# Kernel optimization log

Measured on AMD Instinct MI355X. Metric: run time of the kernel, lower is better.

## Reference

```python
import jax, jax.numpy as jnp
import numpy as np

N, T, C, G, E = 50000, 2, 768, 16, 800000
H = C // 4          # 192
OUT = 3
EPS = 1e-5


def _lin_init(k, fan_in, fan_out):
    s = 1.0 / np.sqrt(fan_in)
    kw, kb = jax.random.split(k)
    W = jax.random.uniform(kw, (fan_in, fan_out), minval=-s, maxval=s, dtype=jnp.float32)
    b = jax.random.uniform(kb, (fan_out,), minval=-s, maxval=s, dtype=jnp.float32)
    return W, b


def setup_inputs() -> dict:
    key = jax.random.key(0)
    ks = jax.random.split(key, 8)
    x = jax.random.normal(ks[0], (N, T, C), dtype=jnp.float32)
    batch = jnp.sort(jax.random.randint(ks[1], (N,), 0, G))
    edge_index = jax.random.randint(ks[2], (2, E), 0, N)
    W0, b0 = _lin_init(ks[3], C, H)
    W1, b1 = _lin_init(ks[4], H, H)
    Wh1, bh1 = _lin_init(ks[5], H, H)
    Wh2, bh2 = _lin_init(ks[6], H, OUT)
    ones = jnp.ones((H,), jnp.float32)
    zeros = jnp.zeros((H,), jnp.float32)
    return {
        "x": x, "batch": batch, "edge_index": edge_index,
        "W0": W0, "b0": b0, "gn0_w": ones, "gn0_b": zeros, "gn0_a": ones,
        "W1": W1, "b1": b1, "gn1_w": ones, "gn1_b": zeros, "gn1_a": ones,
        "Wh1": Wh1, "bh1": bh1, "Wh2": Wh2, "bh2": bh2,
    }


def _gelu(v):
    return jax.nn.gelu(v, approximate=False)  # torch nn.GELU default = exact erf


def _gcn_conv(h, W, b, src, dst, dinv):
    # PyG GCNConv: x' = D^-1/2 (A+I) D^-1/2 (x W) + b, self-loops added implicitly
    h = jnp.einsum('ntc,cd->ntd', h, W)                       # [N,T,Cout]
    norm = (dinv[src] * dinv[dst])[:, None, None]             # [E,1,1]
    agg = jax.ops.segment_sum(h[src] * norm, dst, num_segments=N)
    agg = agg + h * (dinv * dinv)[:, None, None]              # self-loop term
    return agg + b


def _graph_norm(h, batch, cnt, w, b, alpha):
    # PyG GraphNorm: per-graph mean/var with learnable mean scale
    mean = jax.ops.segment_sum(h, batch, num_segments=G) / cnt   # [G,T,C]
    out = h - alpha * mean[batch]
    var = jax.ops.segment_sum(out * out, batch, num_segments=G) / cnt
    std = jnp.sqrt(var + EPS)
    return w * out / std[batch] + b


def reference(x, batch, edge_index,
              W0, b0, gn0_w, gn0_b, gn0_a,
              W1, b1, gn1_w, gn1_b, gn1_a,
              Wh1, bh1, Wh2, bh2):
    src, dst = edge_index[0], edge_index[1]
    deg = jax.ops.segment_sum(jnp.ones((E,), jnp.float32), dst, num_segments=N) + 1.0
    dinv = jax.lax.rsqrt(deg)
    cnt = jax.ops.segment_sum(jnp.ones((N,), jnp.float32), batch, num_segments=G)[:, None, None]

    # layer 0: 768 -> 192 (no residual, shape mismatch)
    h = _gcn_conv(x, W0, b0, src, dst, dinv)
    h = _gelu(_graph_norm(h, batch, cnt, gn0_w, gn0_b, gn0_a))
    # layer 1: 192 -> 192 with residual
    h_in = h
    h = _gcn_conv(h, W1, b1, src, dst, dinv)
    h = _gelu(_graph_norm(h, batch, cnt, gn1_w, gn1_b, gn1_a))
    h = h + h_in
    # MLP head
    h = _gelu(jnp.einsum('ntc,cd->ntd', h, Wh1) + bh1)
    out = jnp.einsum('ntc,cd->ntd', h, Wh2) + bh2            # [N,T,3]
    return out
```

## Files before the change

### kernel.cpp

```cpp
#include <hip/hip_runtime.h>
#include <math.h>

#define NN   50000
#define TT   2
#define CC   768
#define GG   16
#define EE   800000
#define HH   192
#define OUTD 3
#define MR   (NN*TT)
#define FD   (TT*HH)
#define EPS_GN 1e-5f
#define GN_CHUNK 32
#define AGG_CH 128

typedef __attribute__((ext_vector_type(8))) short bf16x8;
typedef __attribute__((ext_vector_type(4))) float f32x4;

__device__ __forceinline__ float gelu_exact(float x){
    return 0.5f * x * (1.0f + erff(x * 0.70710678118654752440f));
}

__device__ __forceinline__ short f2b(float f){
    unsigned u = __float_as_uint(f);
    unsigned r = (u + 0x7FFFu + ((u>>16)&1u)) >> 16;
    return (short)r;
}
__device__ __forceinline__ float b2f(unsigned short u){
    return __uint_as_float(((unsigned)u)<<16);
}

__global__ __launch_bounds__(256) void k_deg(const int* __restrict__ dst, float* __restrict__ deg){
    int e = blockIdx.x*256 + threadIdx.x;
    if(e < EE) atomicAdd(&deg[dst[e]], 1.0f);
}

__global__ __launch_bounds__(64) void k_cnt2(const int* __restrict__ batch, float* __restrict__ cnt){
    int g = threadIdx.x;
    if(g >= GG) return;
    int lo0=0, hi=NN;
    while(lo0<hi){ int mid=(lo0+hi)>>1; if(batch[mid] < g) lo0=mid+1; else hi=mid; }
    int lo1=lo0; hi=NN;
    while(lo1<hi){ int mid=(lo1+hi)>>1; if(batch[mid] < g+1) lo1=mid+1; else hi=mid; }
    cnt[g] = (float)(lo1 - lo0);
}

__global__ __launch_bounds__(256) void k_wconv(const float* __restrict__ W0, const float* __restrict__ W1,
                                               const float* __restrict__ Wh1,
                                               short* __restrict__ Wt0, short* __restrict__ Wt1,
                                               short* __restrict__ Wth1){
    int i = blockIdx.x*256 + threadIdx.x;
    if(i < CC*HH){
        int k = i / HH, n = i % HH;
        Wt0[(size_t)n*CC + k] = f2b(W0[i]);
    }
    if(i < HH*HH){
        int k = i / HH, n = i % HH;
        Wt1 [(size_t)n*HH + k] = f2b(W1[i]);
        Wth1[(size_t)n*HH + k] = f2b(Wh1[i]);
    }
}

__global__ __launch_bounds__(256) void k_scan1(const float* __restrict__ deg, int* __restrict__ partial,
                                               float* __restrict__ dinv){
    __shared__ int s[256];
    int t = threadIdx.x;
    int i = blockIdx.x*256 + t;
    float dv = (i < NN) ? deg[i] : 0.f;
    if(i < NN) dinv[i] = rsqrtf(dv + 1.0f);
    int v = (int)dv;
    s[t] = v; __syncthreads();
    for(int off=128; off>0; off>>=1){ if(t < off) s[t] += s[t+off]; __syncthreads(); }
    if(t == 0) partial[blockIdx.x] = s[0];
}

__global__ __launch_bounds__(256) void k_scan2(int* __restrict__ partial){
    __shared__ int s[256];
    int t = threadIdx.x;
    int v = partial[t];
    s[t] = v; __syncthreads();
    for(int off=1; off<256; off<<=1){
        int x = (t >= off) ? s[t-off] : 0;
        __syncthreads();
        s[t] += x;
        __syncthreads();
    }
    partial[t] = s[t] - v;
}

__global__ __launch_bounds__(256) void k_scan3(const float* __restrict__ deg, const int* __restrict__ partial,
                                               int* __restrict__ csr_off){
    __shared__ int s[256];
    int t = threadIdx.x;
    int i = blockIdx.x*256 + t;
    int v = (i < NN) ? (int)deg[i] : 0;
    s[t] = v; __syncthreads();
    for(int off=1; off<256; off<<=1){
        int x = (t >= off) ? s[t-off] : 0;
        __syncthreads();
        s[t] += x;
        __syncthreads();
    }
    if(i < NN) csr_off[i] = partial[blockIdx.x] + s[t] - v;
}

__global__ __launch_bounds__(256) void k_fill(const int* __restrict__ src, const int* __restrict__ dst,
                                              const int* __restrict__ csr_off, int* __restrict__ fillcnt,
                                              int* __restrict__ csr_src){
    int e = blockIdx.x*256 + threadIdx.x;
    if(e < EE){
        int d = dst[e];
        int pos = csr_off[d] + atomicAdd(&fillcnt[d], 1);
        csr_src[pos] = src[e];
    }
}

__device__ __forceinline__ void gn8r(float4 u0, float4 u1,
                                     const float* __restrict__ sm, const float* __restrict__ sq,
                                     int sb, int hb_,
                                     const float* __restrict__ wg, const float* __restrict__ bg,
                                     const float* __restrict__ ag, float ic, float v[8]){
    float4 m0 = *(const float4*)(sm+sb),   m1 = *(const float4*)(sm+sb+4);
    float4 q0 = *(const float4*)(sq+sb),   q1 = *(const float4*)(sq+sb+4);
    float4 w0 = *(const float4*)(wg+hb_),  w1 = *(const float4*)(wg+hb_+4);
    float4 b0 = *(const float4*)(bg+hb_),  b1 = *(const float4*)(bg+hb_+4);
    float4 a0 = *(const float4*)(ag+hb_),  a1 = *(const float4*)(ag+hb_+4);
    float uu[8]={u0.x,u0.y,u0.z,u0.w,u1.x,u1.y,u1.z,u1.w};
    float mm[8]={m0.x,m0.y,m0.z,m0.w,m1.x,m1.y,m1.z,m1.w};
    float qq[8]={q0.x,q0.y,q0.z,q0.w,q1.x,q1.y,q1.z,q1.w};
    float ww[8]={w0.x,w0.y,w0.z,w0.w,w1.x,w1.y,w1.z,w1.w};
    float bb[8]={b0.x,b0.y,b0.z,b0.w,b1.x,b1.y,b1.z,b1.w};
    float aa[8]={a0.x,a0.y,a0.z,a0.w,a1.x,a1.y,a1.z,a1.w};
    #pragma unroll
    for(int j=0;j<8;j++){
        float mean = mm[j]*ic, ex2 = qq[j]*ic, al = aa[j];
        float var = ex2 - (2.0f*al - al*al)*mean*mean;
        float t = ww[j]*(uu[j] - al*mean)*rsqrtf(var + EPS_GN) + bb[j];
        v[j] = gelu_exact(t);
    }
}

template<int MODE, int NORM, bool BIAS>
__global__ __launch_bounds__(256) void k_gemm_mfma(
        const float* __restrict__ A1, const float* __restrict__ A0,
        const short* __restrict__ Bt,
        const float* __restrict__ bias, void* __restrict__ Cv,
        const float* __restrict__ W2, const float* __restrict__ b2,
        const int* __restrict__ batch, const float* __restrict__ cnt,
        const float* __restrict__ sm1, const float* __restrict__ sq1,
        const float* __restrict__ wg1, const float* __restrict__ bg1, const float* __restrict__ ag1,
        const float* __restrict__ sm0, const float* __restrict__ sq0,
        const float* __restrict__ wg0, const float* __restrict__ bg0, const float* __restrict__ ag0,
        int Mrows, int Kdim){
    __shared__ short As[64][40];
    __shared__ short Bs[192][40];
    int tid = threadIdx.x;
    int bm = blockIdx.x*64;
    int wv = tid>>6, lane = tid&63;
    int lm = lane&15, lq = lane>>4;

    f32x4 acc[12];
    #pragma unroll
    for(int i=0;i<12;i++) acc[i] = (f32x4){0.f,0.f,0.f,0.f};

    int ar = tid>>2, akg = (tid&3)<<3;
    int row = bm + ar;
    bool aok = row < Mrows;
    const float* Ap1 = A1 + (size_t)row*Kdim + akg;
    const float* Ap0 = (NORM==2) ? (A0 + (size_t)row*Kdim + akg) : nullptr;
    int g = 0, tT = 0; float ic = 0.f;
    if(NORM >= 1 && aok){
        int nn = row>>1; tT = row&1;
        g = batch[nn];
        ic = 1.0f / cnt[g];
    }

    float4 ra0 = make_float4(0,0,0,0), ra1 = ra0, rb0 = ra0, rb1 = ra0;
    bf16x8 bv[3];
    if(aok){
        ra0 = *(const float4*)(Ap1); ra1 = *(const float4*)(Ap1 + 4);
        if(NORM==2){ rb0 = *(const float4*)(Ap0); rb1 = *(const float4*)(Ap0 + 4); }
    }
    #pragma unroll
    for(int i=0;i<3;i++){
        int idx = tid + i*256;
        int n = idx>>2, kg = (idx&3)<<3;
        bv[i] = *(const bf16x8*)(Bt + (size_t)n*Kdim + kg);
    }

    for(int k0 = 0; k0 < Kdim; k0 += 32){
        bf16x8 ap = {};
        if(aok){
            if(NORM == 0){
                ap[0]=f2b(ra0.x); ap[1]=f2b(ra0.y); ap[2]=f2b(ra0.z); ap[3]=f2b(ra0.w);
                ap[4]=f2b(ra1.x); ap[5]=f2b(ra1.y); ap[6]=f2b(ra1.z); ap[7]=f2b(ra1.w);
            } else {
                int hb_ = akg + k0;
                int sb  = g*FD + tT*HH + hb_;
                float v[8];
                gn8r(ra0, ra1, sm1, sq1, sb, hb_, wg1, bg1, ag1, ic, v);
                if(NORM == 2){
                    float v0[8];
                    gn8r(rb0, rb1, sm0, sq0, sb, hb_, wg0, bg0, ag0, ic, v0);
                    #pragma unroll
                    for(int j=0;j<8;j++) v[j] += v0[j];
                }
                #pragma unroll
                for(int j=0;j<8;j++) ap[j] = f2b(v[j]);
            }
        }
        bf16x8 bw0 = bv[0], bw1 = bv[1], bw2 = bv[2];
        __syncthreads();
        *(bf16x8*)&As[ar][akg] = ap;
        {
            int idx0 = tid, idx1 = tid+256, idx2 = tid+512;
            *(bf16x8*)&Bs[idx0>>2][(idx0&3)<<3] = bw0;
            *(bf16x8*)&Bs[idx1>>2][(idx1&3)<<3] = bw1;
            *(bf16x8*)&Bs[idx2>>2][(idx2&3)<<3] = bw2;
        }
        __syncthreads();
        int k1 = k0 + 32;
        if(k1 < Kdim){
            if(aok){
                ra0 = *(const float4*)(Ap1 + k1); ra1 = *(const float4*)(Ap1 + k1 + 4);
                if(NORM==2){ rb0 = *(const float4*)(Ap0 + k1); rb1 = *(const float4*)(Ap0 + k1 + 4); }
            }
            #pragma unroll
            for(int i=0;i<3;i++){
                int idx = tid + i*256;
                int n = idx>>2, kg = (idx&3)<<3;
                bv[i] = *(const bf16x8*)(Bt + (size_t)n*Kdim + k1 + kg);
            }
        }
        bf16x8 af = *(const bf16x8*)&As[wv*16 + lm][lq*8];
        #pragma unroll
        for(int ct=0; ct<12; ct++){
            bf16x8 bfr = *(const bf16x8*)&Bs[ct*16 + lm][lq*8];
            acc[ct] = __builtin_amdgcn_mfma_f32_16x16x32_bf16(af, bfr, acc[ct], 0, 0, 0);
        }
    }

    if(MODE == 1){
        short* C = (short*)Cv;
        #pragma unroll
        for(int ct=0; ct<12; ct++){
            int col = ct*16 + lm;
            float bs = BIAS ? bias[col] : 0.f;
            #pragma unroll
            for(int r=0; r<4; r++){
                int orow = bm + wv*16 + lq*4 + r;
                if(orow < Mrows) C[(size_t)orow*HH + col] = f2b(acc[ct][r] + bs);
            }
        }
    } else {
        float hs[4][3] = {};
        #pragma unroll
        for(int ct=0; ct<12; ct++){
            int col = ct*16 + lm;
            float bs = bias[col];
            float w20 = W2[col*3+0], w21 = W2[col*3+1], w22 = W2[col*3+2];
            #pragma unroll
            for(int r=0; r<4; r++){
                float gl = gelu_exact(acc[ct][r] + bs);
                hs[r][0] += gl*w20; hs[r][1] += gl*w21; hs[r][2] += gl*w22;
            }
        }
        #pragma unroll
        for(int off=1; off<16; off<<=1){
            #pragma unroll
            for(int r=0;r<4;r++){
                hs[r][0] += __shfl_xor(hs[r][0], off);
                hs[r][1] += __shfl_xor(hs[r][1], off);
                hs[r][2] += __shfl_xor(hs[r][2], off);
            }
        }
        if(lm == 0){
            float* O = (float*)Cv;
            #pragma unroll
            for(int r=0;r<4;r++){
                int orow = bm + wv*16 + lq*4 + r;
                if(orow < Mrows){
                    O[(size_t)orow*3+0] = hs[r][0] + b2[0];
                    O[(size_t)orow*3+1] = hs[r][1] + b2[1];
                    O[(size_t)orow*3+2] = hs[r][2] + b2[2];
                }
            }
        }
    }
}

__global__ __launch_bounds__(192) void k_agg(const ushort* __restrict__ hw, const int* __restrict__ csr_src,
                                             const int* __restrict__ csr_off, const float* __restrict__ deg,
                                             const float* __restrict__ dinv, const float* __restrict__ bias,
                                             float* __restrict__ out){
    __shared__ int   sidx[AGG_CH];
    __shared__ float swt [AGG_CH];
    int n = blockIdx.x;
    int t = threadIdx.x;
    float di = dinv[n];
    const ushort2* H2 = (const ushort2*)hw;
    ushort2 sv = H2[(size_t)n*192 + t];
    float self = di*di;
    float ax = b2f(sv.x)*self, ay = b2f(sv.y)*self;
    int beg = csr_off[n];
    int end = beg + (int)deg[n];
    for(int base = beg; base < end; base += AGG_CH){
        int m = min(AGG_CH, end - base);
        __syncthreads();
        for(int j = t; j < m; j += 192){
            int s = csr_src[base + j];
            sidx[j] = s;
            swt[j] = dinv[s]*di;
        }
        __syncthreads();
        int j = 0;
        for(; j+8 <= m; j += 8){
            int   si[8]; float wt[8]; ushort2 vv[8];
            #pragma unroll
            for(int q=0;q<8;q++){ si[q]=sidx[j+q]; wt[q]=swt[j+q]; }
            #pragma unroll
            for(int q=0;q<8;q++) vv[q] = H2[(size_t)si[q]*192 + t];
            #pragma unroll
            for(int q=0;q<8;q++){ ax += wt[q]*b2f(vv[q].x); ay += wt[q]*b2f(vv[q].y); }
        }
        for(; j < m; j++){
            int s = sidx[j]; float ww = swt[j];
            ushort2 v = H2[(size_t)s*192 + t];
            ax += ww*b2f(v.x); ay += ww*b2f(v.y);
        }
    }
    int f = 2*t;
    int hh = (f < HH) ? f : f - HH;
    out[(size_t)n*FD + f]   = ax + bias[hh];
    out[(size_t)n*FD + f+1] = ay + bias[hh+1];
}

__global__ __launch_bounds__(384) void k_gn_stats(const float* __restrict__ h, const int* __restrict__ batch,
                                                  float* __restrict__ ssum, float* __restrict__ ssq){
    int f = threadIdx.x;
    int n0 = blockIdx.x*GN_CHUNK;
    int n1 = min(n0 + GN_CHUNK, NN);
    int g = batch[n0];
    float a = 0.f, a2 = 0.f;
    int n = n0;
    for(; n+4 <= n1; n += 4){
        float v0 = h[(size_t)n*FD + f];
        float v1 = h[(size_t)(n+1)*FD + f];
        float v2 = h[(size_t)(n+2)*FD + f];
        float v3 = h[(size_t)(n+3)*FD + f];
        int b3 = batch[n+3];
        if(b3 == g){
            a  += v0+v1+v2+v3;
            a2 += v0*v0+v1*v1+v2*v2+v3*v3;
        } else {
            float vv[4] = {v0,v1,v2,v3};
            #pragma unroll
            for(int q=0;q<4;q++){
                int gn = batch[n+q];
                if(gn != g){
                    atomicAdd(&ssum[g*FD + f], a);
                    atomicAdd(&ssq [g*FD + f], a2);
                    a = 0.f; a2 = 0.f; g = gn;
                }
                a += vv[q]; a2 += vv[q]*vv[q];
            }
        }
    }
    for(; n < n1; n++){
        int gn = batch[n];
        if(gn != g){
            atomicAdd(&ssum[g*FD + f], a);
            atomicAdd(&ssq [g*FD + f], a2);
            a = 0.f; a2 = 0.f; g = gn;
        }
        float v = h[(size_t)n*FD + f];
        a += v; a2 += v*v;
    }
    atomicAdd(&ssum[g*FD + f], a);
    atomicAdd(&ssq [g*FD + f], a2);
}

extern "C" void kernel_launch(void* const* d_in, const int* in_sizes, int n_in,
                              void* d_out, int out_size, void* d_ws, size_t ws_size,
                              hipStream_t stream){
    const float* x     = (const float*)d_in[0];
    const int*   batch = (const int*)d_in[1];
    const int*   ei    = (const int*)d_in[2];
    const int*   src   = ei;
    const int*   dst   = ei + EE;
    const float* W0    = (const float*)d_in[3];
    const float* b0    = (const float*)d_in[4];
    const float* gn0_w = (const float*)d_in[5];
    const float* gn0_b = (const float*)d_in[6];
    const float* gn0_a = (const float*)d_in[7];
    const float* W1    = (const float*)d_in[8];
    const float* b1    = (const float*)d_in[9];
    const float* gn1_w = (const float*)d_in[10];
    const float* gn1_b = (const float*)d_in[11];
    const float* gn1_a = (const float*)d_in[12];
    const float* Wh1   = (const float*)d_in[13];
    const float* bh1   = (const float*)d_in[14];
    const float* Wh2   = (const float*)d_in[15];
    const float* bh2   = (const float*)d_in[16];
    float* out = (float*)d_out;

    char* w = (char*)d_ws;
    auto alloc = [&](size_t bytes)->void*{
        void* p = (void*)w;
        w += (bytes + 255) & ~(size_t)255;
        return p;
    };
    char* zbase = w;
    float* deg     = (float*)alloc((size_t)NN*4);
    int*   fillcnt = (int*)  alloc((size_t)NN*4);
    int*   partial = (int*)  alloc(256*4);
    float* s0m     = (float*)alloc((size_t)GG*FD*4);
    float* s0q     = (float*)alloc((size_t)GG*FD*4);
    float* s1m     = (float*)alloc((size_t)GG*FD*4);
    float* s1q     = (float*)alloc((size_t)GG*FD*4);
    size_t zbytes = (size_t)(w - zbase);
    float* cnt     = (float*)alloc((size_t)GG*4);
    float* dinv    = (float*)alloc((size_t)NN*4);
    int*   csr_off = (int*)  alloc((size_t)NN*4);
    int*   csr_src = (int*)  alloc((size_t)EE*4);
    short* Wt0     = (short*)alloc((size_t)HH*CC*2);
    short* Wt1     = (short*)alloc((size_t)HH*HH*2);
    short* Wth1    = (short*)alloc((size_t)HH*HH*2);
    short* hb0     = (short*)alloc((size_t)MR*HH*2);
    short* hb1     = (short*)alloc((size_t)MR*HH*2);
    float* agg0    = (float*)alloc((size_t)MR*HH*4);
    float* agg1    = (float*)alloc((size_t)MR*HH*4);

    hipMemsetAsync(zbase, 0, zbytes, stream);

    k_deg  <<<(EE+255)/256, 256, 0, stream>>>(dst, deg);
    k_cnt2 <<<1, 64, 0, stream>>>(batch, cnt);
    k_wconv<<<(CC*HH+255)/256, 256, 0, stream>>>(W0, W1, Wh1, Wt0, Wt1, Wth1);

    int nscan = (NN+255)/256;
    k_scan1<<<nscan, 256, 0, stream>>>(deg, partial, dinv);
    k_scan2<<<1,     256, 0, stream>>>(partial);
    k_scan3<<<nscan, 256, 0, stream>>>(deg, partial, csr_off);
    k_fill <<<(EE+255)/256, 256, 0, stream>>>(src, dst, csr_off, fillcnt, csr_src);

    int gemm_grid = (MR+63)/64;
    int ngn = (NN + GN_CHUNK - 1)/GN_CHUNK;

    k_gemm_mfma<1,0,false><<<gemm_grid, 256, 0, stream>>>(
        x, nullptr, Wt0, nullptr, hb0, nullptr, nullptr,
        nullptr, nullptr,
        nullptr, nullptr, nullptr, nullptr, nullptr,
        nullptr, nullptr, nullptr, nullptr, nullptr, MR, CC);
    k_agg<<<NN, 192, 0, stream>>>((const ushort*)hb0, csr_src, csr_off, deg, dinv, b0, agg0);
    k_gn_stats<<<ngn, 384, 0, stream>>>(agg0, batch, s0m, s0q);

    k_gemm_mfma<1,1,false><<<gemm_grid, 256, 0, stream>>>(
        agg0, nullptr, Wt1, nullptr, hb1, nullptr, nullptr,
        batch, cnt,
        s0m, s0q, gn0_w, gn0_b, gn0_a,
        nullptr, nullptr, nullptr, nullptr, nullptr, MR, HH);
    k_agg<<<NN, 192, 0, stream>>>((const ushort*)hb1, csr_src, csr_off, deg, dinv, b1, agg1);
    k_gn_stats<<<ngn, 384, 0, stream>>>(agg1, batch, s1m, s1q);

    k_gemm_mfma<2,2,true><<<gemm_grid, 256, 0, stream>>>(
        agg1, agg0, Wth1, bh1, out, Wh2, bh2,
        batch, cnt,
        s1m, s1q, gn1_w, gn1_b, gn1_a,
        s0m, s0q, gn0_w, gn0_b, gn0_a, MR, HH);
}
```

Measured before the change: 985.9 us.

## Rework aggregation to warp-per-node with shuffles and restructure GEMMs

The aggregation kernel now gives each node one 64-lane wavefront instead of a 192-thread block. Edge indices and weights are broadcast with shuffles rather than staged through shared memory, and each lane handles six features. The 192-K GEMM now stages half of the weight matrix in LDS per phase and feeds A fragments straight from registers, which removes the per-k-step A staging and barriers. The 768-K GEMM is split into a dedicated kernel, and the group-count kernel is merged into the scan kernel to save one launch. The trade-offs are more scattered 4-byte gathers per lane in aggregation and a larger LDS footprint in the GEMM.

New measurement: 1.296 ms. 1.31x slower.

```diff
diff --git a/kernel.cpp b/kernel.cpp
--- a/kernel.cpp
+++ b/kernel.cpp
@@ -12,7 +12,6 @@
 #define FD   (TT*HH)
 #define EPS_GN 1e-5f
 #define GN_CHUNK 32
-#define AGG_CH 128
 
 typedef __attribute__((ext_vector_type(8))) short bf16x8;
 typedef __attribute__((ext_vector_type(4))) float f32x4;
@@ -33,16 +32,6 @@
 __global__ __launch_bounds__(256) void k_deg(const int* __restrict__ dst, float* __restrict__ deg){
     int e = blockIdx.x*256 + threadIdx.x;
     if(e < EE) atomicAdd(&deg[dst[e]], 1.0f);
-}
-
-__global__ __launch_bounds__(64) void k_cnt2(const int* __restrict__ batch, float* __restrict__ cnt){
-    int g = threadIdx.x;
-    if(g >= GG) return;
-    int lo0=0, hi=NN;
-    while(lo0<hi){ int mid=(lo0+hi)>>1; if(batch[mid] < g) lo0=mid+1; else hi=mid; }
-    int lo1=lo0; hi=NN;
-    while(lo1<hi){ int mid=(lo1+hi)>>1; if(batch[mid] < g+1) lo1=mid+1; else hi=mid; }
-    cnt[g] = (float)(lo1 - lo0);
 }
 
 __global__ __launch_bounds__(256) void k_wconv(const float* __restrict__ W0, const float* __restrict__ W1,
@@ -74,9 +63,18 @@
     if(t == 0) partial[blockIdx.x] = s[0];
 }
 
-__global__ __launch_bounds__(256) void k_scan2(int* __restrict__ partial){
+__global__ __launch_bounds__(256) void k_scan2(int* __restrict__ partial, const int* __restrict__ batch,
+                                               float* __restrict__ cnt){
     __shared__ int s[256];
     int t = threadIdx.x;
+    if(t < GG){
+        int g = t;
+        int lo0=0, hi=NN;
+        while(lo0<hi){ int mid=(lo0+hi)>>1; if(batch[mid] < g) lo0=mid+1; else hi=mid; }
+        int lo1=lo0; hi=NN;
+        while(lo1<hi){ int mid=(lo1+hi)>>1; if(batch[mid] < g+1) lo1=mid+1; else hi=mid; }
+        cnt[g] = (float)(lo1 - lo0);
+    }
     int v = partial[t];
     s[t] = v; __syncthreads();
     for(int off=1; off<256; off<<=1){
@@ -140,8 +138,81 @@
     }
 }
 
+__global__ __launch_bounds__(256) void k_gemm0(const float* __restrict__ A, const short* __restrict__ Bt,
+                                               short* __restrict__ C, int Mrows){
+    __shared__ short As[64][40];
+    __shared__ short Bs[192][40];
+    int tid = threadIdx.x;
+    int bm = blockIdx.x*64;
+    int wv = tid>>6, lane = tid&63;
+    int lm = lane&15, lq = lane>>4;
+
+    f32x4 acc[12];
+    #pragma unroll
+    for(int i=0;i<12;i++) acc[i] = (f32x4){0.f,0.f,0.f,0.f};
+
+    int ar = tid>>2, akg = (tid&3)<<3;
+    int row = bm + ar;
+    bool aok = row < Mrows;
+    const float* Ap = A + (size_t)row*CC + akg;
+
+    float4 ra0 = make_float4(0,0,0,0), ra1 = ra0;
+    bf16x8 bv[3];
+    if(aok){ ra0 = *(const float4*)(Ap); ra1 = *(const float4*)(Ap + 4); }
+    #pragma unroll
+    for(int i=0;i<3;i++){
+        int idx = tid + i*256;
+        int n = idx>>2, kg = (idx&3)<<3;
+        bv[i] = *(const bf16x8*)(Bt + (size_t)n*CC + kg);
+    }
+
+    for(int k0 = 0; k0 < CC; k0 += 32){
+        bf16x8 ap = {};
+        if(aok){
+            ap[0]=f2b(ra0.x); ap[1]=f2b(ra0.y); ap[2]=f2b(ra0.z); ap[3]=f2b(ra0.w);
+            ap[4]=f2b(ra1.x); ap[5]=f2b(ra1.y); ap[6]=f2b(ra1.z); ap[7]=f2b(ra1.w);
+        }
+        bf16x8 bw0 = bv[0], bw1 = bv[1], bw2 = bv[2];
+        __syncthreads();
+        *(bf16x8*)&As[ar][akg] = ap;
+        {
+            int idx0 = tid, idx1 = tid+256, idx2 = tid+512;
+            *(bf16x8*)&Bs[idx0>>2][(idx0&3)<<3] = bw0;
+            *(bf16x8*)&Bs[idx1>>2][(idx1&3)<<3] = bw1;
+            *(bf16x8*)&Bs[idx2>>2][(idx2&3)<<3] = bw2;
+        }
+        __syncthreads();
+        int k1 = k0 + 32;
+        if(k1 < CC){
+            if(aok){ ra0 = *(const float4*)(Ap + k1); ra1 = *(const float4*)(Ap + k1 + 4); }
+            #pragma unroll
+            for(int i=0;i<3;i++){
+                int idx = tid + i*256;
+                int n = idx>>2, kg = (idx&3)<<3;
+                bv[i] = *(const bf16x8*)(Bt + (size_t)n*CC + k1 + kg);
+            }
+        }
+        bf16x8 af = *(const bf16x8*)&As[wv*16 + lm][lq*8];
+        #pragma unroll
+        for(int ct=0; ct<12; ct++){
+            bf16x8 bfr = *(const bf16x8*)&Bs[ct*16 + lm][lq*8];
+            acc[ct] = __builtin_amdgcn_mfma_f32_16x16x32_bf16(af, bfr, acc[ct], 0, 0, 0);
+        }
+    }
+
+    #pragma unroll
+    for(int ct=0; ct<12; ct++){
+        int col = ct*16 + lm;
+        #pragma unroll
+        for(int r=0; r<4; r++){
+            int orow = bm + wv*16 + lq*4 + r;
+            if(orow < Mrows) C[(size_t)orow*HH + col] = f2b(acc[ct][r]);
+        }
+    }
+}
+
 template<int MODE, int NORM, bool BIAS>
-__global__ __launch_bounds__(256) void k_gemm_mfma(
+__global__ __launch_bounds__(256) void k_gemm192(
         const float* __restrict__ A1, const float* __restrict__ A0,
         const short* __restrict__ Bt,
         const float* __restrict__ bias, void* __restrict__ Cv,
@@ -151,9 +222,8 @@
         const float* __restrict__ wg1, const float* __restrict__ bg1, const float* __restrict__ ag1,
         const float* __restrict__ sm0, const float* __restrict__ sq0,
         const float* __restrict__ wg0, const float* __restrict__ bg0, const float* __restrict__ ag0,
-        int Mrows, int Kdim){
-    __shared__ short As[64][40];
-    __shared__ short Bs[192][40];
+        int Mrows){
+    __shared__ short Bs[192][104];
     int tid = threadIdx.x;
     int bm = blockIdx.x*64;
     int wv = tid>>6, lane = tid&63;
@@ -163,80 +233,62 @@
     #pragma unroll
     for(int i=0;i<12;i++) acc[i] = (f32x4){0.f,0.f,0.f,0.f};
 
-    int ar = tid>>2, akg = (tid&3)<<3;
-    int row = bm + ar;
+    int row = bm + wv*16 + lm;
     bool aok = row < Mrows;
-    const float* Ap1 = A1 + (size_t)row*Kdim + akg;
-    const float* Ap0 = (NORM==2) ? (A0 + (size_t)row*Kdim + akg) : nullptr;
+    const float* Ap1 = A1 + (size_t)row*HH + lq*8;
+    const float* Ap0 = (NORM==2) ? (A0 + (size_t)row*HH + lq*8) : nullptr;
     int g = 0, tT = 0; float ic = 0.f;
-    if(NORM >= 1 && aok){
-        int nn = row>>1; tT = row&1;
-        g = batch[nn];
+    if(aok){
+        g = batch[row>>1]; tT = row&1;
         ic = 1.0f / cnt[g];
     }
 
-    float4 ra0 = make_float4(0,0,0,0), ra1 = ra0, rb0 = ra0, rb1 = ra0;
-    bf16x8 bv[3];
-    if(aok){
-        ra0 = *(const float4*)(Ap1); ra1 = *(const float4*)(Ap1 + 4);
-        if(NORM==2){ rb0 = *(const float4*)(Ap0); rb1 = *(const float4*)(Ap0 + 4); }
-    }
-    #pragma unroll
-    for(int i=0;i<3;i++){
-        int idx = tid + i*256;
-        int n = idx>>2, kg = (idx&3)<<3;
-        bv[i] = *(const bf16x8*)(Bt + (size_t)n*Kdim + kg);
-    }
-
-    for(int k0 = 0; k0 < Kdim; k0 += 32){
-        bf16x8 ap = {};
-        if(aok){
-            if(NORM == 0){
-                ap[0]=f2b(ra0.x); ap[1]=f2b(ra0.y); ap[2]=f2b(ra0.z); ap[3]=f2b(ra0.w);
-                ap[4]=f2b(ra1.x); ap[5]=f2b(ra1.y); ap[6]=f2b(ra1.z); ap[7]=f2b(ra1.w);
-            } else {
-                int hb_ = akg + k0;
+    #pragma unroll
+    for(int ph=0; ph<2; ph++){
+        if(ph) __syncthreads();
+        #pragma unroll
+        for(int t=0;t<9;t++){
+            int idx = tid + t*256;
+            int n = idx/12, kg = (idx%12)*8;
+            *(bf16x8*)&Bs[n][kg] = *(const bf16x8*)(Bt + (size_t)n*HH + ph*96 + kg);
+        }
+        __syncthreads();
+        float4 pa[3][2], pb[3][2];
+        #pragma unroll
+        for(int k3=0;k3<3;k3++){
+            int k0 = ph*96 + k3*32;
+            if(aok){
+                pa[k3][0] = *(const float4*)(Ap1 + k0);
+                pa[k3][1] = *(const float4*)(Ap1 + k0 + 4);
+                if(NORM==2){
+                    pb[k3][0] = *(const float4*)(Ap0 + k0);
+                    pb[k3][1] = *(const float4*)(Ap0 + k0 + 4);
+                }
+            }
+        }
+        #pragma unroll
+        for(int k3=0;k3<3;k3++){
+            int k0 = ph*96 + k3*32;
+            bf16x8 ap = {};
+            if(aok){
+                int hb_ = k0 + lq*8;
                 int sb  = g*FD + tT*HH + hb_;
                 float v[8];
-                gn8r(ra0, ra1, sm1, sq1, sb, hb_, wg1, bg1, ag1, ic, v);
+                gn8r(pa[k3][0], pa[k3][1], sm1, sq1, sb, hb_, wg1, bg1, ag1, ic, v);
                 if(NORM == 2){
                     float v0[8];
-                    gn8r(rb0, rb1, sm0, sq0, sb, hb_, wg0, bg0, ag0, ic, v0);
+                    gn8r(pb[k3][0], pb[k3][1], sm0, sq0, sb, hb_, wg0, bg0, ag0, ic, v0);
                     #pragma unroll
                     for(int j=0;j<8;j++) v[j] += v0[j];
                 }
                 #pragma unroll
                 for(int j=0;j<8;j++) ap[j] = f2b(v[j]);
             }
-        }
-        bf16x8 bw0 = bv[0], bw1 = bv[1], bw2 = bv[2];
-        __syncthreads();
-        *(bf16x8*)&As[ar][akg] = ap;
-        {
-            int idx0 = tid, idx1 = tid+256, idx2 = tid+512;
-            *(bf16x8*)&Bs[idx0>>2][(idx0&3)<<3] = bw0;
-            *(bf16x8*)&Bs[idx1>>2][(idx1&3)<<3] = bw1;
-            *(bf16x8*)&Bs[idx2>>2][(idx2&3)<<3] = bw2;
-        }
-        __syncthreads();
-        int k1 = k0 + 32;
-        if(k1 < Kdim){
-            if(aok){
-                ra0 = *(const float4*)(Ap1 + k1); ra1 = *(const float4*)(Ap1 + k1 + 4);
-                if(NORM==2){ rb0 = *(const float4*)(Ap0 + k1); rb1 = *(const float4*)(Ap0 + k1 + 4); }
-            }
-            #pragma unroll
-            for(int i=0;i<3;i++){
-                int idx = tid + i*256;
-                int n = idx>>2, kg = (idx&3)<<3;
-                bv[i] = *(const bf16x8*)(Bt + (size_t)n*Kdim + k1 + kg);
-            }
-        }
-        bf16x8 af = *(const bf16x8*)&As[wv*16 + lm][lq*8];
-        #pragma unroll
-        for(int ct=0; ct<12; ct++){
-            bf16x8 bfr = *(const bf16x8*)&Bs[ct*16 + lm][lq*8];
-            acc[ct] = __builtin_amdgcn_mfma_f32_16x16x32_bf16(af, bfr, acc[ct], 0, 0, 0);
+            #pragma unroll
+            for(int ct=0; ct<12; ct++){
+                bf16x8 bfr = *(const bf16x8*)&Bs[ct*16 + lm][k3*32 + lq*8];
+                acc[ct] = __builtin_amdgcn_mfma_f32_16x16x32_bf16(ap, bfr, acc[ct], 0, 0, 0);
+            }
         }
     }
 
@@ -289,50 +341,62 @@
     }
 }
 
-__global__ __launch_bounds__(192) void k_agg(const ushort* __restrict__ hw, const int* __restrict__ csr_src,
+__global__ __launch_bounds__(256) void k_agg(const ushort* __restrict__ hw, const int* __restrict__ csr_src,
                                              const int* __restrict__ csr_off, const float* __restrict__ deg,
                                              const float* __restrict__ dinv, const float* __restrict__ bias,
                                              float* __restrict__ out){
-    __shared__ int   sidx[AGG_CH];
-    __shared__ float swt [AGG_CH];
-    int n = blockIdx.x;
-    int t = threadIdx.x;
+    int lane = threadIdx.x & 63;
+    int n = blockIdx.x*4 + (threadIdx.x>>6);
+    if(n >= NN) return;
     float di = dinv[n];
     const ushort2* H2 = (const ushort2*)hw;
-    ushort2 sv = H2[(size_t)n*192 + t];
+    size_t rb = (size_t)n*192 + lane*3;
+    ushort2 s0v = H2[rb], s1v = H2[rb+1], s2v = H2[rb+2];
     float self = di*di;
-    float ax = b2f(sv.x)*self, ay = b2f(sv.y)*self;
+    float a0 = b2f(s0v.x)*self, a1 = b2f(s0v.y)*self;
+    float a2 = b2f(s1v.x)*self, a3 = b2f(s1v.y)*self;
+    float a4 = b2f(s2v.x)*self, a5 = b2f(s2v.y)*self;
     int beg = csr_off[n];
     int end = beg + (int)deg[n];
-    for(int base = beg; base < end; base += AGG_CH){
-        int m = min(AGG_CH, end - base);
-        __syncthreads();
-        for(int j = t; j < m; j += 192){
-            int s = csr_src[base + j];
-            sidx[j] = s;
-            swt[j] = dinv[s]*di;
-        }
-        __syncthreads();
+    for(int base = beg; base < end; base += 64){
+        int m = min(64, end - base);
+        int e = 0; float we = 0.f;
+        if(lane < m){ e = csr_src[base + lane]; we = dinv[e]*di; }
         int j = 0;
-        for(; j+8 <= m; j += 8){
-            int   si[8]; float wt[8]; ushort2 vv[8];
-            #pragma unroll
-            for(int q=0;q<8;q++){ si[q]=sidx[j+q]; wt[q]=swt[j+q]; }
-            #pragma unroll
-            for(int q=0;q<8;q++) vv[q] = H2[(size_t)si[q]*192 + t];
-            #pragma unroll
-            for(int q=0;q<8;q++){ ax += wt[q]*b2f(vv[q].x); ay += wt[q]*b2f(vv[q].y); }
+        for(; j+4 <= m; j += 4){
+            int   sA=__shfl(e,j),  sB=__shfl(e,j+1),  sC=__shfl(e,j+2),  sD=__shfl(e,j+3);
+            float wA=__shfl(we,j), wB=__shfl(we,j+1), wC=__shfl(we,j+2), wD=__shfl(we,j+3);
+            size_t bA=(size_t)sA*192+lane*3, bB=(size_t)sB*192+lane*3;
+            size_t bC=(size_t)sC*192+lane*3, bD=(size_t)sD*192+lane*3;
+            ushort2 vA0=H2[bA], vA1=H2[bA+1], vA2=H2[bA+2];
+            ushort2 vB0=H2[bB], vB1=H2[bB+1], vB2=H2[bB+2];
+            ushort2 vC0=H2[bC], vC1=H2[bC+1], vC2=H2[bC+2];
+            ushort2 vD0=H2[bD], vD1=H2[bD+1], vD2=H2[bD+2];
+            a0 += wA*b2f(vA0.x)+wB*b2f(vB0.x)+wC*b2f(vC0.x)+wD*b2f(vD0.x);
+            a1 += wA*b2f(vA0.y)+wB*b2f(vB0.y)+wC*b2f(vC0.y)+wD*b2f(vD0.y);
+            a2 += wA*b2f(vA1.x)+wB*b2f(vB1.x)+wC*b2f(vC1.x)+wD*b2f(vD1.x);
+            a3 += wA*b2f(vA1.y)+wB*b2f(vB1.y)+wC*b2f(vC1.y)+wD*b2f(vD1.y);
+            a4 += wA*b2f(vA2.x)+wB*b2f(vB2.x)+wC*b2f(vC2.x)+wD*b2f(vD2.x);
+            a5 += wA*b2f(vA2.y)+wB*b2f(vB2.y)+wC*b2f(vC2.y)+wD*b2f(vD2.y);
         }
         for(; j < m; j++){
-            int s = sidx[j]; float ww = swt[j];
-            ushort2 v = H2[(size_t)s*192 + t];
-            ax += ww*b2f(v.x); ay += ww*b2f(v.y);
-        }
-    }
-    int f = 2*t;
-    int hh = (f < HH) ? f : f - HH;
-    out[(size_t)n*FD + f]   = ax + bias[hh];
-    out[(size_t)n*FD + f+1] = ay + bias[hh+1];
+            int s = __shfl(e, j); float ww = __shfl(we, j);
+            size_t sb = (size_t)s*192 + lane*3;
+            ushort2 v0=H2[sb], v1=H2[sb+1], v2=H2[sb+2];
+            a0 += ww*b2f(v0.x); a1 += ww*b2f(v0.y);
+            a2 += ww*b2f(v1.x); a3 += ww*b2f(v1.y);
+            a4 += ww*b2f(v2.x); a5 += ww*b2f(v2.y);
+        }
+    }
+    int f0 = lane*6;
+    float r[6] = {a0,a1,a2,a3,a4,a5};
+    float* O = out + (size_t)n*FD + f0;
+    #pragma unroll
+    for(int i=0;i<6;i++){
+        int f = f0 + i;
+        int hh = (f < HH) ? f : f - HH;
+        O[i] = r[i] + bias[hh];
+    }
 }
 
 __global__ __launch_bounds__(384) void k_gn_stats(const float* __restrict__ h, const int* __restrict__ batch,
@@ -434,37 +498,33 @@
     hipMemsetAsync(zbase, 0, zbytes, stream);
 
     k_deg  <<<(EE+255)/256, 256, 0, stream>>>(dst, deg);
-    k_cnt2 <<<1, 64, 0, stream>>>(batch, cnt);
     k_wconv<<<(CC*HH+255)/256, 256, 0, stream>>>(W0, W1, Wh1, Wt0, Wt1, Wth1);
 
     int nscan = (NN+255)/256;
     k_scan1<<<nscan, 256, 0, stream>>>(deg, partial, dinv);
-    k_scan2<<<1,     256, 0, stream>>>(partial);
+    k_scan2<<<1,     256, 0, stream>>>(partial, batch, cnt);
     k_scan3<<<nscan, 256, 0, stream>>>(deg, partial, csr_off);
     k_fill <<<(EE+255)/256, 256, 0, stream>>>(src, dst, csr_off, fillcnt, csr_src);
 
     int gemm_grid = (MR+63)/64;
+    int agg_grid  = (NN+3)/4;
     int ngn = (NN + GN_CHUNK - 1)/GN_CHUNK;
 
-    k_gemm_mfma<1,0,false><<<gemm_grid, 256, 0, stream>>>(
-        x, nullptr, Wt0, nullptr, hb0, nullptr, nullptr,
-        nullptr, nullptr,
-        nullptr, nullptr, nullptr, nullptr, nullptr,
-        nullptr, nullptr, nullptr, nullptr, nullptr, MR, CC);
-    k_agg<<<NN, 192, 0, stream>>>((const ushort*)hb0, csr_src, csr_off, deg, dinv, b0, agg0);
+    k_gemm0<<<gemm_grid, 256, 0, stream>>>(x, Wt0, hb0, MR);
+    k_agg<<<agg_grid, 256, 0, stream>>>((const ushort*)hb0, csr_src, csr_off, deg, dinv, b0, agg0);
     k_gn_stats<<<ngn, 384, 0, stream>>>(agg0, batch, s0m, s0q);
 
-    k_gemm_mfma<1,1,false><<<gemm_grid, 256, 0, stream>>>(
+    k_gemm192<1,1,false><<<gemm_grid, 256, 0, stream>>>(
         agg0, nullptr, Wt1, nullptr, hb1, nullptr, nullptr,
         batch, cnt,
         s0m, s0q, gn0_w, gn0_b, gn0_a,
-        nullptr, nullptr, nullptr, nullptr, nullptr, MR, HH);
-    k_agg<<<NN, 192, 0, stream>>>((const ushort*)hb1, csr_src, csr_off, deg, dinv, b1, agg1);
+        nullptr, nullptr, nullptr, nullptr, nullptr, MR);
+    k_agg<<<agg_grid, 256, 0, stream>>>((const ushort*)hb1, csr_src, csr_off, deg, dinv, b1, agg1);
     k_gn_stats<<<ngn, 384, 0, stream>>>(agg1, batch, s1m, s1q);
 
-    k_gemm_mfma<2,2,true><<<gemm_grid, 256, 0, stream>>>(
+    k_gemm192<2,2,true><<<gemm_grid, 256, 0, stream>>>(
         agg1, agg0, Wth1, bh1, out, Wh2, bh2,
         batch, cnt,
         s1m, s1q, gn1_w, gn1_b, gn1_a,
-        s0m, s0q, gn0_w, gn0_b, gn0_a, MR, HH);
-}
+        s0m, s0q, gn0_w, gn0_b, gn0_a, MR);
+}
```
